# Kernel tuning notes

Hardware: AMD Instinct MI355X
Metric: run time of the kernel (lower is better)

Reference implementation:

```python
import jax, jax.numpy as jnp
import numpy as np

N = 32768          # total nodes
C = 384            # in/out channels == embed_dim
E = 384            # embed_dim
G = 12             # tetrahedral group size
H = 1              # effective_num_heads = num_heads // G
D = 32             # head_dim = (E // G) // H
P = D // 2         # RoPE rotation pairs
SD = 3             # spatial dims
NUM_GRAPHS = 64
AVG_NUM_NODES = float(N) / NUM_GRAPHS  # 512.0, passed as avg_num_nodes


def rope_apply(t, phase):
    # t: [N,G,H,D], phase: [N,G,H,P]; rotate consecutive (even,odd) pairs
    c, s = jnp.cos(phase), jnp.sin(phase)
    t2 = t.reshape(*t.shape[:-1], P, 2)
    x1, x2 = t2[..., 0], t2[..., 1]
    rot = jnp.stack([x1 * c - x2 * s, x1 * s + x2 * c], axis=-1)
    return rot.reshape(t.shape)


def setup_inputs() -> dict:
    key = jax.random.key(0)
    ks = jax.random.split(key, 8)
    x = jax.random.normal(ks[0], (N, C), jnp.float32)
    pos = jax.random.normal(ks[1], (N, SD), jnp.float32)
    batch = jnp.sort(jax.random.randint(ks[2], (N,), 0, NUM_GRAPHS)).astype(jnp.int32)
    sc = 1.0 / np.sqrt(C).astype(np.float32)
    Wq = jax.random.normal(ks[3], (C, E), jnp.float32) * sc
    Wv = jax.random.normal(ks[4], (C, E), jnp.float32) * sc
    Wo = jax.random.normal(ks[5], (E, C), jnp.float32) * (1.0 / np.sqrt(E).astype(np.float32))
    freqs = jax.random.normal(ks[6], (G, H, P, SD), jnp.float32)  # freq_sigma = 1.0
    return {
        'x': x, 'pos': pos, 'batch': batch,
        'Wq': Wq, 'bq': jnp.zeros((E,), jnp.float32),
        'Wv': Wv, 'bv': jnp.zeros((E,), jnp.float32),
        'Wo': Wo, 'bo': jnp.zeros((C,), jnp.float32),
        'freqs': freqs,
    }


def reference(x, pos, batch, Wq, bq, Wv, bv, Wo, bo, freqs):
    # projections -> [N, G, H, D]
    q = (x @ Wq + bq).reshape(N, G, H, D)
    v = (x @ Wv + bv).reshape(N, G, H, D)
    # RoPE phase from positions: [N, G, H, P]
    phase = jnp.einsum('ns,ghps->nghp', pos, freqs)
    q = rope_apply(q, phase)
    k = rope_apply(jnp.ones_like(q), phase)  # use_key=False -> k_raw = ones
    # linear attention: per-node outer product, then per-graph segment sum
    kv = jnp.einsum('nghd,nghe->nghde', k, v)              # [N,G,H,D,D]
    kv_kernel = jax.ops.segment_sum(kv, batch, num_segments=NUM_GRAPHS)
    kv_kernel = kv_kernel / AVG_NUM_NODES                  # mean_aggregation=False
    out = jnp.einsum('nghd,nghde->nghe', q, kv_kernel[batch])
    out = out.reshape(N, -1)
    return out @ Wo + bo
```

## Files before the change

kernel.cpp:

```cpp
#include <hip/hip_runtime.h>


#define N_NODES 32768
#define K_DIM   384
#define P_PAIR  16
#define NUM_GRAPHS 64

typedef unsigned short u16;
typedef __bf16 bf16x8 __attribute__((ext_vector_type(8)));
typedef float  f32x4  __attribute__((ext_vector_type(4)));
typedef __attribute__((address_space(3))) void       lds_void;
typedef const __attribute__((address_space(1))) void gbl_void;

__device__ __forceinline__ u16 f2bf(float f) {
    unsigned int i = __float_as_uint(f);
    unsigned int r = i + 0x7FFFu + ((i >> 16) & 1u);
    return (u16)(r >> 16);
}
__device__ __forceinline__ float bf2f(u16 u) {
    union { unsigned int i; float f; } x;
    x.i = ((unsigned int)u) << 16;
    return x.f;
}

__global__ void prep(const float* __restrict__ x,
                     const float* __restrict__ Wq, const float* __restrict__ Wv,
                     const float* __restrict__ Wo,
                     u16* __restrict__ xb, u16* __restrict__ WqvT,
                     u16* __restrict__ WoT) {
    int b = blockIdx.x;
    if (b < 6144) {
        int i = (b * 256 + threadIdx.x) * 8;
        float4 a0 = *reinterpret_cast<const float4*>(x + i);
        float4 a1 = *reinterpret_cast<const float4*>(x + i + 4);
        union { u16 u[8]; float4 v; } pk;
        pk.u[0] = f2bf(a0.x); pk.u[1] = f2bf(a0.y);
        pk.u[2] = f2bf(a0.z); pk.u[3] = f2bf(a0.w);
        pk.u[4] = f2bf(a1.x); pk.u[5] = f2bf(a1.y);
        pk.u[6] = f2bf(a1.z); pk.u[7] = f2bf(a1.w);
        *reinterpret_cast<float4*>(xb + i) = pk.v;
    } else {
        int idx = (b - 6144) * 256 + threadIdx.x;
        if (idx < 294912) {
            int n = idx / 384, k = idx % 384;
            WqvT[idx] = f2bf(n < 384 ? Wq[k * 384 + n] : Wv[k * 384 + (n - 384)]);
        } else {
            int j = idx - 294912;
            int n = j / 384, k = j % 384;
            WoT[j] = f2bf(Wo[k * 384 + n]);
        }
    }
}

#define GEMM_CORE(A_PTR, B_PTR)                                                  \
    __shared__ __align__(1024) u16 T[8192];                                      \
    const int tid = threadIdx.x;                                                 \
    const int w = tid >> 6, lane = tid & 63;                                     \
    const int wr = (w >> 1) << 6, wc = (w & 1) << 6;                             \
    const int lm = lane & 15, q = lane >> 4;                                     \
    const int srow = lane >> 2, sc8 = (lane & 3) << 3;                           \
    f32x4 acc[4][4];                                                             \
    _Pragma("unroll") for (int i = 0; i < 4; i++)                                \
    _Pragma("unroll") for (int j = 0; j < 4; j++)                                \
    _Pragma("unroll") for (int r = 0; r < 4; r++) acc[i][j][r] = 0.0f;           \
    for (int k0 = 0; k0 < K_DIM; k0 += 32) {                                     \
        __syncthreads();                                                         \
        _Pragma("unroll")                                                        \
        for (int s = w; s < 16; s += 4) {                                        \
            int row = ((s & 7) << 4) + srow;                                     \
            const u16* gp = ((s >> 3) ? (B_PTR) + (size_t)(n0 + row) * K_DIM     \
                                      : (A_PTR) + (size_t)(m0 + row) * K_DIM)    \
                            + k0 + sc8;                                          \
            __builtin_amdgcn_global_load_lds((gbl_void*)gp,                      \
                                             (lds_void*)&T[s << 9], 16, 0, 0);   \
        }                                                                        \
        __syncthreads();                                                         \
        bf16x8 af[4], bfr[4];                                                    \
        _Pragma("unroll") for (int i = 0; i < 4; i++) {                          \
            af[i]  = *reinterpret_cast<const bf16x8*>(&T[(wr + i * 16 + lm) * 32 + q * 8]);          \
            bfr[i] = *reinterpret_cast<const bf16x8*>(&T[4096 + (wc + i * 16 + lm) * 32 + q * 8]);   \
        }                                                                        \
        _Pragma("unroll") for (int i = 0; i < 4; i++)                            \
        _Pragma("unroll") for (int j = 0; j < 4; j++)                            \
            acc[i][j] = __builtin_amdgcn_mfma_f32_16x16x32_bf16(af[i], bfr[j], acc[i][j], 0, 0, 0);  \
    }

__global__ __launch_bounds__(256) void gemm_qv(
    const u16* __restrict__ A, const u16* __restrict__ Bt,
    const float* __restrict__ bq, const float* __restrict__ bv,
    u16* __restrict__ Qw, u16* __restrict__ Vd) {
    const int b = blockIdx.x;
    const int xcd = b & 7, jj = b >> 3;
    const int by = xcd * 32 + jj / 6, bx = jj % 6;
    const int m0 = by << 7, n0 = bx << 7;
    GEMM_CORE(A, Bt)
    u16* Cq = (n0 < 384) ? Qw : Vd;
    const float* bias = (n0 < 384) ? bq : bv;
    const int coff = (n0 < 384) ? 0 : 384;
#pragma unroll
    for (int j = 0; j < 4; j++) {
        int gc = n0 + wc + j * 16 + lm - coff;
        float bs = bias[gc];
#pragma unroll
        for (int i = 0; i < 4; i++) {
            int gr = m0 + wr + i * 16 + q * 4;
#pragma unroll
            for (int r = 0; r < 4; r++)
                Cq[(size_t)(gr + r) * 384 + gc] = f2bf(acc[i][j][r] + bs);
        }
    }
}

__global__ __launch_bounds__(256) void gemm_out(
    const u16* __restrict__ A, const u16* __restrict__ Bt,
    const float* __restrict__ bias, float* __restrict__ Cmat) {
    const int b = blockIdx.x;
    const int xcd = b & 7, jj = b >> 3;
    const int by = xcd * 32 + jj / 3, bx = jj % 3;
    const int m0 = by << 7, n0 = bx << 7;
    GEMM_CORE(A, Bt)
#pragma unroll
    for (int j = 0; j < 4; j++) {
        int gc = n0 + wc + j * 16 + lm;
        float bs = bias[gc];
#pragma unroll
        for (int i = 0; i < 4; i++) {
            int gr = m0 + wr + i * 16 + q * 4;
#pragma unroll
            for (int r = 0; r < 4; r++)
                Cmat[(size_t)(gr + r) * 384 + gc] = acc[i][j][r] + bs;
        }
    }
}

__global__ __launch_bounds__(384) void kv_k(
    const u16* __restrict__ V, const float* __restrict__ pos,
    const int* __restrict__ batch, const float* __restrict__ freqs,
    float* __restrict__ KV) {
    const int nb = blockIdx.x << 6;
    const int t = threadIdx.x;
    const int grp = t >> 5, ec = t & 31;
    const int p = ec >> 1, sgn = ec & 1;
    const float f0 = freqs[(grp * P_PAIR + p) * 3 + 0];
    const float f1 = freqs[(grp * P_PAIR + p) * 3 + 1];
    const float f2 = freqs[(grp * P_PAIR + p) * 3 + 2];

    __shared__ float kbuf[8][384];
    __shared__ int gbuf[8];
    float acc[32];
#pragma unroll
    for (int d = 0; d < 32; d++) acc[d] = 0.0f;
    int gcur = batch[nb];
    const float scale = 1.0f / 512.0f;

    for (int base = nb; base < nb + 64; base += 8) {
        __syncthreads();
        if (t < 8) gbuf[t] = batch[base + t];
#pragma unroll
        for (int i = 0; i < 8; i++) {
            int n = base + i;
            float ph = pos[n * 3 + 0] * f0 + pos[n * 3 + 1] * f1 + pos[n * 3 + 2] * f2;
            float sn, cs;
            __sincosf(ph, &sn, &cs);
            kbuf[i][t] = sgn ? (sn + cs) : (cs - sn);
        }
        __syncthreads();
#pragma unroll
        for (int i = 0; i < 8; i++) {
            int g = gbuf[i];
            if (g != gcur) {
                float* dst = KV + ((gcur * 12 + grp) << 10) + ec;
#pragma unroll
                for (int d = 0; d < 32; d++) {
                    atomicAdd(dst + (d << 5), acc[d] * scale);
                    acc[d] = 0.0f;
                }
                gcur = g;
            }
            float vv = bf2f(V[(size_t)(base + i) * 384 + t]);
            const float* kr = &kbuf[i][grp << 5];
#pragma unroll
            for (int d = 0; d < 32; d++) acc[d] = fmaf(kr[d], vv, acc[d]);
        }
    }
    float* dst = KV + ((gcur * 12 + grp) << 10) + ec;
#pragma unroll
    for (int d = 0; d < 32; d++) atomicAdd(dst + (d << 5), acc[d] * scale);
}

__global__ __launch_bounds__(384) void attn_k(
    u16* __restrict__ Qw, const float* __restrict__ pos,
    const int* __restrict__ batch, const float* __restrict__ freqs,
    const float* __restrict__ KV) {
    const int nb = blockIdx.x << 6;
    const int t = threadIdx.x;
    const int grp = t >> 5, ec = t & 31;
    const int p = ec >> 1, sgn = ec & 1;
    const float f0 = freqs[(grp * P_PAIR + p) * 3 + 0];
    const float f1 = freqs[(grp * P_PAIR + p) * 3 + 1];
    const float f2 = freqs[(grp * P_PAIR + p) * 3 + 2];

    __shared__ float qbuf[8][384];
    __shared__ int gbuf[8];
    float kv[32];
    int gcur = -1;
    const int cq = t & ~1;

    for (int base = nb; base < nb + 64; base += 8) {
        __syncthreads();
        if (t < 8) gbuf[t] = batch[base + t];
#pragma unroll
        for (int i = 0; i < 8; i++) {
            int n = base + i;
            float qa = bf2f(Qw[(size_t)n * 384 + cq]);
            float qb = bf2f(Qw[(size_t)n * 384 + cq + 1]);
            float ph = pos[n * 3 + 0] * f0 + pos[n * 3 + 1] * f1 + pos[n * 3 + 2] * f2;
            float sn, cs;
            __sincosf(ph, &sn, &cs);
            qbuf[i][t] = sgn ? (qa * sn + qb * cs) : (qa * cs - qb * sn);
        }
        __syncthreads();
#pragma unroll
        for (int i = 0; i < 8; i++) {
            int g = gbuf[i];
            if (g != gcur) {
                gcur = g;
                const float* src = KV + ((g * 12 + grp) << 10) + ec;
#pragma unroll
                for (int d = 0; d < 32; d++) kv[d] = src[d << 5];
            }
            const float* qr = &qbuf[i][grp << 5];
            float o = 0.0f;
#pragma unroll
            for (int d = 0; d < 32; d++) o = fmaf(qr[d], kv[d], o);
            Qw[(size_t)(base + i) * 384 + t] = f2bf(o);
        }
    }
}

extern "C" void kernel_launch(void* const* d_in, const int* in_sizes, int n_in,
                              void* d_out, int out_size, void* d_ws, size_t ws_size,
                              hipStream_t stream) {
    const float* x     = (const float*)d_in[0];
    const float* pos   = (const float*)d_in[1];
    const int*   batch = (const int*)d_in[2];
    const float* Wq    = (const float*)d_in[3];
    const float* bq    = (const float*)d_in[4];
    const float* Wv    = (const float*)d_in[5];
    const float* bv    = (const float*)d_in[6];
    const float* Wo    = (const float*)d_in[7];
    const float* bo    = (const float*)d_in[8];
    const float* fr    = (const float*)d_in[9];
    float* out = (float*)d_out;

    char* ws = (char*)d_ws;
    float* KV   = (float*)(ws);
    u16*   WqvT = (u16*)(ws + 3145728);
    u16*   WoT  = (u16*)(ws + 3735552);
    u16*   Qw   = (u16*)(ws + 4030464);
    u16*   Vd   = (u16*)d_out;
    u16*   xb   = (u16*)d_out + N_NODES * 384;

    hipMemsetAsync(KV, 0, (size_t)NUM_GRAPHS * 12 * 32 * 32 * sizeof(float), stream);
    prep<<<dim3(7872), dim3(256), 0, stream>>>(x, Wq, Wv, Wo, xb, WqvT, WoT);
    gemm_qv<<<dim3(1536), dim3(256), 0, stream>>>(xb, WqvT, bq, bv, Qw, Vd);
    kv_k<<<dim3(512), dim3(384), 0, stream>>>(Vd, pos, batch, fr, KV);
    attn_k<<<dim3(512), dim3(384), 0, stream>>>(Qw, pos, batch, fr, KV);
    gemm_out<<<dim3(768), dim3(256), 0, stream>>>(Qw, WoT, bo, out);
}
```

Before: 243.8 us.

## Compute per-graph KV with MFMA blocks per (graph,group) and drop atomics

Replaces the node-chunked scalar-FMA kv kernel with one block per (graph, group) that finds its segment by binary search over the sorted batch array. Each block builds the RoPE key in bf16, stages V via global_load_lds, and accumulates k^T v with 32x32x16 bf16 MFMA. Four waves are reduced in LDS and written directly, which removes the atomics and the memset. This lowers the key precision to bf16 and relies on batch being sorted. Load balance now follows graph sizes.

```diff
diff --git a/kernel.cpp b/kernel.cpp
--- a/kernel.cpp
+++ b/kernel.cpp
@@ -9,6 +9,7 @@
 typedef unsigned short u16;
 typedef __bf16 bf16x8 __attribute__((ext_vector_type(8)));
 typedef float  f32x4  __attribute__((ext_vector_type(4)));
+typedef float  f32x16 __attribute__((ext_vector_type(16)));
 typedef __attribute__((address_space(3))) void       lds_void;
 typedef const __attribute__((address_space(1))) void gbl_void;
 
@@ -133,59 +134,88 @@
     }
 }
 
-__global__ __launch_bounds__(384) void kv_k(
+__global__ __launch_bounds__(256) void kv_mfma(
     const u16* __restrict__ V, const float* __restrict__ pos,
     const int* __restrict__ batch, const float* __restrict__ freqs,
     float* __restrict__ KV) {
-    const int nb = blockIdx.x << 6;
-    const int t = threadIdx.x;
-    const int grp = t >> 5, ec = t & 31;
-    const int p = ec >> 1, sgn = ec & 1;
+    const int bid = blockIdx.x;
+    const int xcd = bid & 7, jj = bid >> 3;
+    const int g = (xcd << 3) + jj / 12, grp = jj % 12;
+
+    const int tid = threadIdx.x;
+    const int w = tid >> 6, lane = tid & 63;
+    const int hi = lane >> 5, de = lane & 31;
+    const int p = de >> 1, sgn = de & 1;
+
     const float f0 = freqs[(grp * P_PAIR + p) * 3 + 0];
     const float f1 = freqs[(grp * P_PAIR + p) * 3 + 1];
     const float f2 = freqs[(grp * P_PAIR + p) * 3 + 2];
 
-    __shared__ float kbuf[8][384];
-    __shared__ int gbuf[8];
-    float acc[32];
-#pragma unroll
-    for (int d = 0; d < 32; d++) acc[d] = 0.0f;
-    int gcur = batch[nb];
-    const float scale = 1.0f / 512.0f;
-
-    for (int base = nb; base < nb + 64; base += 8) {
-        __syncthreads();
-        if (t < 8) gbuf[t] = batch[base + t];
-#pragma unroll
-        for (int i = 0; i < 8; i++) {
-            int n = base + i;
-            float ph = pos[n * 3 + 0] * f0 + pos[n * 3 + 1] * f1 + pos[n * 3 + 2] * f2;
+    int s0 = 0, s1 = N_NODES;
+    while (s0 < s1) { int m = (s0 + s1) >> 1; if (batch[m] < g) s0 = m + 1; else s1 = m; }
+    const int start = s0;
+    int e0 = start, e1 = N_NODES;
+    while (e0 < e1) { int m = (e0 + e1) >> 1; if (batch[m] < g + 1) e0 = m + 1; else e1 = m; }
+    const int end = e0;
+
+    __shared__ __align__(1024) u16 vbuf[2048];
+    __shared__ float posb[192];
+    __shared__ __align__(16) float red[4096];
+
+    f32x16 acc;
+#pragma unroll
+    for (int r = 0; r < 16; r++) acc[r] = 0.0f;
+
+    const int nl0 = w * 16 + hi * 8;
+
+    for (int c = start; c < end; c += 64) {
+        __syncthreads();
+        if (tid < 192) {
+            int i = c * 3 + tid;
+            posb[tid] = (i < 3 * N_NODES) ? pos[i] : 0.0f;
+        }
+        {
+            int r = tid >> 2;
+            int nn = c + r;
+            const u16* gp = V + (size_t)nn * K_DIM + (grp << 5) + ((tid & 3) << 3);
+            if (nn < N_NODES)
+                __builtin_amdgcn_global_load_lds((gbl_void*)gp,
+                                                 (lds_void*)&vbuf[w << 9], 16, 0, 0);
+        }
+        __syncthreads();
+
+        union { bf16x8 v; u16 u[8]; } A, B;
+#pragma unroll
+        for (int j = 0; j < 8; j++) {
+            int nl = nl0 + j;
+            int n = c + nl;
+            float ph = posb[nl * 3 + 0] * f0 + posb[nl * 3 + 1] * f1
+                     + posb[nl * 3 + 2] * f2;
             float sn, cs;
             __sincosf(ph, &sn, &cs);
-            kbuf[i][t] = sgn ? (sn + cs) : (cs - sn);
-        }
-        __syncthreads();
-#pragma unroll
-        for (int i = 0; i < 8; i++) {
-            int g = gbuf[i];
-            if (g != gcur) {
-                float* dst = KV + ((gcur * 12 + grp) << 10) + ec;
-#pragma unroll
-                for (int d = 0; d < 32; d++) {
-                    atomicAdd(dst + (d << 5), acc[d] * scale);
-                    acc[d] = 0.0f;
-                }
-                gcur = g;
-            }
-            float vv = bf2f(V[(size_t)(base + i) * 384 + t]);
-            const float* kr = &kbuf[i][grp << 5];
-#pragma unroll
-            for (int d = 0; d < 32; d++) acc[d] = fmaf(kr[d], vv, acc[d]);
-        }
-    }
-    float* dst = KV + ((gcur * 12 + grp) << 10) + ec;
-#pragma unroll
-    for (int d = 0; d < 32; d++) atomicAdd(dst + (d << 5), acc[d] * scale);
+            float kd = sgn ? (sn + cs) : (cs - sn);
+            bool valid = n < end;
+            A.u[j] = valid ? f2bf(kd) : (u16)0;
+            B.u[j] = valid ? vbuf[(nl << 5) + de] : (u16)0;
+        }
+        acc = __builtin_amdgcn_mfma_f32_32x32x16_bf16(A.v, B.v, acc, 0, 0, 0);
+    }
+
+#pragma unroll
+    for (int r = 0; r < 16; r++) {
+        int d = (r & 3) + ((r >> 2) << 3) + (hi << 2);
+        red[(w << 10) + (d << 5) + de] = acc[r];
+    }
+    __syncthreads();
+    {
+        int i4 = tid << 2;
+        f32x4 a0 = *reinterpret_cast<const f32x4*>(&red[i4]);
+        f32x4 a1 = *reinterpret_cast<const f32x4*>(&red[1024 + i4]);
+        f32x4 a2 = *reinterpret_cast<const f32x4*>(&red[2048 + i4]);
+        f32x4 a3 = *reinterpret_cast<const f32x4*>(&red[3072 + i4]);
+        f32x4 s = (a0 + a1 + a2 + a3) * (1.0f / 512.0f);
+        *reinterpret_cast<f32x4*>(&KV[((size_t)(g * 12 + grp) << 10) + i4]) = s;
+    }
 }
 
 __global__ __launch_bounds__(384) void attn_k(
@@ -261,10 +291,9 @@
     u16*   Vd   = (u16*)d_out;
     u16*   xb   = (u16*)d_out + N_NODES * 384;
 
-    hipMemsetAsync(KV, 0, (size_t)NUM_GRAPHS * 12 * 32 * 32 * sizeof(float), stream);
     prep<<<dim3(7872), dim3(256), 0, stream>>>(x, Wq, Wv, Wo, xb, WqvT, WoT);
     gemm_qv<<<dim3(1536), dim3(256), 0, stream>>>(xb, WqvT, bq, bv, Qw, Vd);
-    kv_k<<<dim3(512), dim3(384), 0, stream>>>(Vd, pos, batch, fr, KV);
+    kv_mfma<<<dim3(768), dim3(256), 0, stream>>>(Vd, pos, batch, fr, KV);
     attn_k<<<dim3(512), dim3(384), 0, stream>>>(Qw, pos, batch, fr, KV);
     gemm_out<<<dim3(768), dim3(256), 0, stream>>>(Qw, WoT, bo, out);
 }
```

Result: faster. 219.2 us (-10.1%).
